# Optimization experiments

Hardware: AMD Instinct MI355X
Metric: run time of the kernel (lower is better)

Reference implementation:

```python
import jax, jax.numpy as jnp
import numpy as np

T, B, COV, H, L = 512, 256, 128, 512, 2
N_DIST_PARAMS = 2  # lnormal


def setup_inputs() -> dict:
    key = jax.random.key(0)
    ks = jax.random.split(key, 20)
    d = {}
    d["x"] = jax.random.normal(ks[0], (T, B, COV + 1), jnp.float32)
    lengths = jax.random.randint(ks[1], (B,), 2, T + 1)
    lengths = -jnp.sort(-lengths)  # packed sequences: descending lengths
    lengths = lengths.at[0].set(T)  # ensure max length == T
    d["lengths"] = lengths
    d["h0"] = jax.random.normal(ks[2], (L, B, H), jnp.float32)
    s = 1.0 / np.sqrt(H)
    in_dims = [COV + 1, H]
    for l in range(L):
        d[f"Wih{l}"] = jax.random.uniform(ks[3 + 4 * l], (3 * H, in_dims[l]), jnp.float32, -s, s)
        d[f"Whh{l}"] = jax.random.uniform(ks[4 + 4 * l], (3 * H, H), jnp.float32, -s, s)
        d[f"bih{l}"] = jax.random.uniform(ks[5 + 4 * l], (3 * H,), jnp.float32, -s, s)
        d[f"bhh{l}"] = jax.random.uniform(ks[6 + 4 * l], (3 * H,), jnp.float32, -s, s)
    sc = 1.0 / np.sqrt(H + 1)
    d["W_cov"] = jax.random.uniform(ks[11], (COV, H + 1), jnp.float32, -sc, sc)
    d["b_cov"] = jax.random.uniform(ks[12], (COV,), jnp.float32, -sc, sc)
    sp = 1.0 / np.sqrt(L * H)
    d["W_par"] = jax.random.uniform(ks[13], (N_DIST_PARAMS, L * H), jnp.float32, -sp, sp)
    d["b_par"] = jax.random.uniform(ks[14], (N_DIST_PARAMS,), jnp.float32, -sp, sp)
    return d


def gru_layer(x, h0, lengths, Wih, Whh, bih, bhh):
    # x: [T, B, D]; h0: [B, H]. PyTorch GRU gate math, masked for ragged lengths
    gi = jnp.einsum('tbd,gd->tbg', x, Wih) + bih  # [T, B, 3H], one big GEMM
    tt = jnp.arange(x.shape[0])

    def step(h, inp):
        gi_t, t = inp
        gh = h @ Whh.T + bhh
        i_r, i_z, i_n = jnp.split(gi_t, 3, axis=-1)
        h_r, h_z, h_n = jnp.split(gh, 3, axis=-1)
        r = jax.nn.sigmoid(i_r + h_r)
        z = jax.nn.sigmoid(i_z + h_z)
        n = jnp.tanh(i_n + r * h_n)
        h_new = (1.0 - z) * n + z * h
        valid = (t < lengths)[:, None]
        h = jnp.where(valid, h_new, h)          # freeze carry past length
        out = jnp.where(valid, h_new, 0.0)       # pad_packed_sequence zero-pads
        return h, out

    h_last, outs = jax.lax.scan(step, h0, (gi, tt))
    return outs, h_last


def reference(x, lengths, h0, Wih0, Whh0, bih0, bhh0, Wih1, Whh1, bih1, bhh1, W_cov, b_cov, W_par, b_par):
    o0, hl0 = gru_layer(x, h0[0], lengths, Wih0, Whh0, bih0, bhh0)
    o1, hl1 = gru_layer(o0, h0[1], lengths, Wih1, Whh1, bih1, bhh1)
    hs = jnp.transpose(o1, (1, 0, 2))  # [B, T, H]
    times = x[:, :, 0].T               # [B, T]
    hwt = jnp.concatenate([hs, times[..., None]], axis=-1)  # [B, T, H+1]
    Tm = x.shape[0]
    # batched masked matmul replacing per-(batch, timestep) GEMV loop
    preds = jnp.einsum('bth,ch->btc', hwt[:, :Tm - 1], W_cov) + b_cov  # [B, T-1, COV]
    mask = (jnp.arange(Tm - 1)[None, :] < (lengths - 1)[:, None])[..., None]
    preds = jnp.where(mask, preds, 0.0)
    # original writes COV values into a COV+1 wide zero buffer; last channel stays 0
    preds = jnp.concatenate([preds, jnp.zeros(preds.shape[:2] + (1,), preds.dtype)], axis=-1)
    last_hidden = jnp.stack([hl0, hl1])                      # [L, B, H]
    last_flat = jnp.reshape(last_hidden, (last_hidden.shape[1], -1))  # torch .view semantics
    dist_params = last_flat @ W_par.T + b_par
    return preds, jnp.exp(-dist_params)
```

## Files before the change

kernel.cpp:

```cpp
#include <hip/hip_runtime.h>


typedef unsigned short u16;
typedef unsigned long long u64;
typedef __attribute__((ext_vector_type(8))) short short8;
typedef short8 bf16x8;
typedef __attribute__((ext_vector_type(4))) float f32x4;

#define T_DIM 512
#define B_DIM 256
#define H_DIM 512
#define G3H   1536
#define BT    131072
#define XPK   256
#define PRED_ELEMS 16875264

#define GLD16(gp, lp) __builtin_amdgcn_global_load_lds( \
    (const __attribute__((address_space(1))) void*)(gp), \
    (__attribute__((address_space(3))) void*)(lp), 16, 0, 0)

__device__ __forceinline__ u16 f2bf(float f) {
    union { float f; unsigned i; } v; v.f = f;
    unsigned i = v.i;
    return (u16)((i + 0x7FFFu + ((i >> 16) & 1u)) >> 16);
}
__device__ __forceinline__ float bf2f(u16 u) {
    union { unsigned i; float f; } v; v.i = ((unsigned)u) << 16; return v.f;
}
__device__ __forceinline__ float sigm(float x) { return 1.f / (1.f + __expf(-x)); }
__device__ __forceinline__ float tanh_f(float x) {
    float ax = fabsf(x);
    float e = __expf(-2.f * ax);
    float t = (1.f - e) / (1.f + e);
    return x < 0.f ? -t : t;
}
__device__ __forceinline__ bf16x8 aload16(const u16* p) {
    union { bf16x8 v; u64 q[2]; } r;
    const u64* qp = (const u64*)p;
    r.q[0] = __hip_atomic_load(qp + 0, __ATOMIC_RELAXED, __HIP_MEMORY_SCOPE_AGENT);
    r.q[1] = __hip_atomic_load(qp + 1, __ATOMIC_RELAXED, __HIP_MEMORY_SCOPE_AGENT);
    return r.v;
}
__device__ __forceinline__ unsigned chk8(bf16x8 v) {
    union { bf16x8 v; unsigned d[4]; } u; u.v = v;
    unsigned b = 0;
#pragma unroll
    for (int i = 0; i < 4; ++i) {
        unsigned d = u.d[i] ^ 0x7FC07FC0u;
        b |= (unsigned)((d & 0xFFFFu) == 0u) | (unsigned)((d >> 16) == 0u);
    }
    return b;
}

__global__ void prep_kernel(const float* __restrict__ Wih0, const float* __restrict__ Wih1,
                            const float* __restrict__ Whh0, const float* __restrict__ Whh1,
                            const float* __restrict__ h0,   const float* __restrict__ Wcov,
                            const float* __restrict__ x,
                            u16* __restrict__ wih0b, u16* __restrict__ wih1b,
                            u16* __restrict__ whh0b, u16* __restrict__ whh1b,
                            u16* __restrict__ h0bf,  u16* __restrict__ wcovb,
                            float* __restrict__ wlastf, u16* __restrict__ xbfc,
                            u16* __restrict__ o0c, u16* __restrict__ o1c, int TC) {
    const int gid = blockIdx.x * 256 + threadIdx.x;
    const int gsz = gridDim.x * 256;
    for (int i = gid; i < 128; i += gsz) wlastf[i] = Wcov[i * 513 + 512];
    for (int i = gid; i < 128 * 512; i += gsz) {
        int r = i >> 9, c = i & 511;
        wcovb[i] = f2bf(Wcov[r * 513 + c]);
    }
    for (int i = gid; i < 512 * 512; i += gsz) h0bf[i] = f2bf(h0[i]);
    for (int i = gid; i < 1536 * XPK; i += gsz) {
        int r = i >> 8, c = i & 255;
        wih0b[i] = f2bf(c < 129 ? Wih0[r * 129 + c] : 0.f);
    }
    for (int i = gid; i < 1536 * 512; i += gsz) wih1b[i] = f2bf(Wih1[i]);
    for (int i = gid; i < 1536 * 512; i += gsz) whh0b[i] = f2bf(Whh0[i]);
    for (int i = gid; i < 1536 * 512; i += gsz) whh1b[i] = f2bf(Whh1[i]);
    {
        const int n = TC * 256 * 256;
        for (int i = gid; i < n; i += gsz) {
            const int row = i >> 8, col = i & 255;
            float v = (col < 129) ? x[(size_t)row * 129 + col] : 0.f;
            xbfc[i] = f2bf(v);
        }
    }
    const u64 SQ = 0x7FC07FC07FC07FC0ULL;
    const size_t nq = (size_t)TC * BT / 4;
    u64* p0 = (u64*)o0c;
    u64* p1 = (u64*)o1c;
    for (size_t i = gid; i < nq; i += gsz) p0[i] = SQ;
    for (size_t i = gid; i < nq; i += gsz) p1[i] = SQ;
}

__global__ void sentinel_kernel(u16* __restrict__ buf, int TC) {
    const u64 SQ = 0x7FC07FC07FC07FC0ULL;
    const size_t nq = (size_t)TC * BT / 4;
    u64* p = (u64*)buf;
    const size_t gid = blockIdx.x * 256 + threadIdx.x;
    const size_t gsz = (size_t)gridDim.x * 256;
    for (size_t i = gid; i < nq; i += gsz) p[i] = SQ;
}

__global__ void cvt_pad_x_kernel(const float* __restrict__ src,
                                 u16* __restrict__ dst, int rows) {
    const int n = rows * 256;
    for (int idx = blockIdx.x * blockDim.x + threadIdx.x; idx < n;
         idx += gridDim.x * blockDim.x) {
        const int row = idx >> 8, col = idx & 255;
        float v = (col < 129) ? src[(size_t)row * 129 + col] : 0.f;
        dst[idx] = f2bf(v);
    }
}

template<int AK>
__global__ __launch_bounds__(256, 2) void scan_fused_kernel(
    const u16* __restrict__ xin,
    const u16* __restrict__ Wih,
    const float* __restrict__ bih,
    const u16* __restrict__ Whh,
    const float* __restrict__ bhh,
    const int* __restrict__ lengths,
    const float* __restrict__ h0l,
    const u16* __restrict__ h0bfl,
    u16* __restrict__ o,
    u16* __restrict__ hcarry,
    float* __restrict__ hlast,
    int t0, int TC) {
    __shared__ __attribute__((aligned(16))) u16 Wl[48 * 520];
    __shared__ __attribute__((aligned(16))) float P[16 * 256];
    __shared__ __attribute__((aligned(16))) float bRZ[32], bNX[16], bNH[16];
    const int tid = threadIdx.x, lane = tid & 63, w = tid >> 6;
    const int n0 = blockIdx.x * 16, b0 = blockIdx.y * 16;
    const int am = lane & 15, aq = lane >> 4;
    constexpr int KW = AK / 4;
    constexpr int KB2 = KW / 32;
#pragma unroll
    for (int it = 0; it < 12; ++it) {
        int f = it * 2048 + tid * 8;
        int j = f >> 9, k = f & 511;
        *(short8*)&Wl[j * 520 + k] =
            *(const short8*)(Whh + ((size_t)((j >> 4) * 512 + n0 + (j & 15))) * 512 + k);
    }
    if (tid < 32) bRZ[tid] = bih[(tid >> 4) * 512 + n0 + (tid & 15)] +
                             bhh[(tid >> 4) * 512 + n0 + (tid & 15)];
    else if (tid < 48) bNX[tid - 32] = bih[1024 + n0 + (tid - 32)];
    else if (tid < 64) bNH[tid - 48] = bhh[1024 + n0 + (tid - 48)];
    bf16x8 wf[3][KB2];
#pragma unroll
    for (int g = 0; g < 3; ++g)
#pragma unroll
        for (int kb = 0; kb < KB2; ++kb)
            wf[g][kb] = *(const short8*)(Wih +
                (size_t)(g * 512 + n0 + am) * AK + w * KW + kb * 32 + aq * 8);
    const int m = tid >> 4, c = tid & 15;
    const int b = b0 + m, col = n0 + c;
    float h = (t0 == 0) ? h0l[(size_t)b * 512 + col]
                        : hlast[(size_t)b * 512 + col];
    const int len = lengths[b];
    bf16x8 xa[KB2], xn[KB2];
#pragma unroll
    for (int kb = 0; kb < KB2; ++kb)
        xa[kb] = *(const short8*)(xin + (size_t)(b0 + am) * AK + w * KW + kb * 32 + aq * 8);
    __syncthreads();
    for (int tl = 0; tl < TC; ++tl) {
        const int t = t0 + tl;
        const u16* Asrc = (tl == 0) ? ((t0 == 0) ? h0bfl : hcarry)
                                    : (o + (size_t)(tl - 1) * BT);
        const u16* arow = Asrc + (size_t)(b0 + am) * 512 + w * 128 + aq * 8;
        bf16x8 av[4];
        if (tl == 0) {
            av[0] = aload16(arow);      av[1] = aload16(arow + 32);
            av[2] = aload16(arow + 64); av[3] = aload16(arow + 96);
        } else {
            for (;;) {
                av[0] = aload16(arow);
                if (!__any((int)chk8(av[0]))) break;
                __builtin_amdgcn_s_sleep(1);
            }
            for (;;) {
                av[1] = aload16(arow + 32);
                av[2] = aload16(arow + 64);
                av[3] = aload16(arow + 96);
                if (!__any((int)(chk8(av[1]) | chk8(av[2]) | chk8(av[3])))) break;
                __builtin_amdgcn_s_sleep(1);
            }
        }
        f32x4 ar = {}, az = {}, anx = {}, anh = {};
#pragma unroll
        for (int kb = 0; kb < KB2; ++kb) {
            ar  = __builtin_amdgcn_mfma_f32_16x16x32_bf16(xa[kb], wf[0][kb], ar, 0, 0, 0);
            az  = __builtin_amdgcn_mfma_f32_16x16x32_bf16(xa[kb], wf[1][kb], az, 0, 0, 0);
            anx = __builtin_amdgcn_mfma_f32_16x16x32_bf16(xa[kb], wf[2][kb], anx, 0, 0, 0);
        }
#pragma unroll
        for (int kb = 0; kb < 4; ++kb) {
            const int k = w * 128 + kb * 32 + aq * 8;
            bf16x8 wr = *(short8*)&Wl[(0 + am) * 520 + k];
            bf16x8 wz = *(short8*)&Wl[(16 + am) * 520 + k];
            bf16x8 wn = *(short8*)&Wl[(32 + am) * 520 + k];
            ar  = __builtin_amdgcn_mfma_f32_16x16x32_bf16(av[kb], wr, ar, 0, 0, 0);
            az  = __builtin_amdgcn_mfma_f32_16x16x32_bf16(av[kb], wz, az, 0, 0, 0);
            anh = __builtin_amdgcn_mfma_f32_16x16x32_bf16(av[kb], wn, anh, 0, 0, 0);
        }
        if (tl < TC - 1) {
#pragma unroll
            for (int kb = 0; kb < KB2; ++kb)
                xn[kb] = *(const short8*)(xin +
                    ((size_t)(tl + 1) * 256 + b0 + am) * AK + w * KW + kb * 32 + aq * 8);
        }
#pragma unroll
        for (int r = 0; r < 4; ++r) {
            P[(w * 4 + 0) * 256 + (aq * 4 + r) * 16 + am] = ar[r];
            P[(w * 4 + 1) * 256 + (aq * 4 + r) * 16 + am] = az[r];
            P[(w * 4 + 2) * 256 + (aq * 4 + r) * 16 + am] = anx[r];
            P[(w * 4 + 3) * 256 + (aq * 4 + r) * 16 + am] = anh[r];
        }
        __syncthreads();
        float Cr = bRZ[c], Cz = bRZ[16 + c], Nx = bNX[c], Nh = bNH[c];
#pragma unroll
        for (int w2 = 0; w2 < 4; ++w2) {
            Cr += P[(w2 * 4 + 0) * 256 + tid];
            Cz += P[(w2 * 4 + 1) * 256 + tid];
            Nx += P[(w2 * 4 + 2) * 256 + tid];
            Nh += P[(w2 * 4 + 3) * 256 + tid];
        }
        __syncthreads();
        float r_ = sigm(Cr);
        float z_ = sigm(Cz);
        float n_ = tanh_f(Nx + r_ * Nh);
        float hnew = (1.f - z_) * n_ + z_ * h;
        h = (t < len) ? hnew : h;
        unsigned hb = (unsigned)f2bf(h);
        unsigned part = hb | ((unsigned)__shfl_down((int)hb, 1) << 16);
        unsigned hi2 = (unsigned)__shfl_down((int)part, 2);
        if ((lane & 3) == 0) {
            u64 q = (u64)part | ((u64)hi2 << 32);
            const int mrow = w * 4 + (lane >> 4);
            const int cg = lane & 15;
            __hip_atomic_store(
                (u64*)(o + (size_t)tl * BT + (size_t)(b0 + mrow) * 512 + n0 + cg),
                q, __ATOMIC_RELAXED, __HIP_MEMORY_SCOPE_AGENT);
        }
        if (tl < TC - 1) {
#pragma unroll
            for (int kb = 0; kb < KB2; ++kb) xa[kb] = xn[kb];
        } else {
            hcarry[(size_t)b * 512 + col] = f2bf(h);
            hlast[(size_t)b * 512 + col] = h;
        }
    }
}

__global__ __launch_bounds__(256) void preds_kernel(
    const u16* __restrict__ o1c, const u16* __restrict__ WcovBf,
    const float* __restrict__ wlastf, const float* __restrict__ bcov,
    const float* __restrict__ x, const int* __restrict__ lengths,
    float* __restrict__ out, int t0) {
    __shared__ __attribute__((aligned(16))) u16 Sh[2][16384];
    const int tid = threadIdx.x, lane = tid & 63, w = tid >> 6;
    const int m0 = blockIdx.x * 128;
    const int r0 = (w & 1) * 64, c0 = (w >> 1) * 64;
    const int am = lane & 15, aq = lane >> 4;
    const int l8 = lane >> 3, lc = lane & 7;
    const int swz = (lc ^ l8) << 3;
    f32x4 acc[4][4] = {};
#pragma unroll
    for (int s = 0; s < 4; ++s) {
        const int i = w * 4 + s, row = i * 8 + l8;
        GLD16(o1c + (size_t)(m0 + row) * 512 + swz, &Sh[0][i * 512]);
        GLD16(WcovBf + (size_t)row * 512 + swz, &Sh[0][8192 + i * 512]);
    }
    __syncthreads();
    int cur = 0;
    for (int kt = 0; kt < 8; ++kt) {
        if (kt + 1 < 8) {
            const int kb = (kt + 1) << 6;
#pragma unroll
            for (int s = 0; s < 4; ++s) {
                const int i = w * 4 + s, row = i * 8 + l8;
                GLD16(o1c + (size_t)(m0 + row) * 512 + kb + swz,
                      &Sh[cur ^ 1][i * 512]);
                GLD16(WcovBf + (size_t)row * 512 + kb + swz,
                      &Sh[cur ^ 1][8192 + i * 512]);
            }
        }
        const u16* Ash = &Sh[cur][0];
        const u16* Bsh = &Sh[cur][8192];
#pragma unroll
        for (int ks = 0; ks < 2; ++ks) {
            bf16x8 a[4], bb[4];
#pragma unroll
            for (int f = 0; f < 4; ++f) {
                const int ar2 = r0 + f * 16 + am;
                a[f] = *(short8*)&Ash[ar2 * 64 + (((ks * 4 + aq) ^ (ar2 & 7)) << 3)];
            }
#pragma unroll
            for (int f = 0; f < 4; ++f) {
                const int br = c0 + f * 16 + am;
                bb[f] = *(short8*)&Bsh[br * 64 + (((ks * 4 + aq) ^ (br & 7)) << 3)];
            }
#pragma unroll
            for (int fi = 0; fi < 4; ++fi)
#pragma unroll
                for (int fj = 0; fj < 4; ++fj)
                    acc[fi][fj] = __builtin_amdgcn_mfma_f32_16x16x32_bf16(
                        a[fi], bb[fj], acc[fi][fj], 0, 0, 0);
        }
        __syncthreads();
        cur ^= 1;
    }
    const int tl = m0 >> 8;
    const int t = t0 + tl;
    if (t < 511) {
#pragma unroll
        for (int fj = 0; fj < 4; ++fj) {
            const int cc = c0 + fj * 16 + am;
            const float bc = bcov[cc], wl = wlastf[cc];
#pragma unroll
            for (int fi = 0; fi < 4; ++fi) {
#pragma unroll
                for (int r = 0; r < 4; ++r) {
                    const int row = m0 + r0 + fi * 16 + aq * 4 + r;
                    const int b = row & 255;
                    const bool valid = t < lengths[b] - 1;
                    const float tim = x[(size_t)t * (256 * 129) + b * 129];
                    out[(size_t)b * (511 * 129) + (size_t)t * 129 + cc] =
                        valid ? acc[fi][fj][r] + bc + tim * wl : 0.f;
                }
            }
        }
        if (tid < 128)
            out[(size_t)((m0 & 255) + tid) * (511 * 129) + (size_t)t * 129 + 128] = 0.f;
    }
}

__global__ void dist_kernel(const float* __restrict__ hl0,
                            const float* __restrict__ hl1,
                            const float* __restrict__ Wpar,
                            const float* __restrict__ bpar, float* __restrict__ out) {
    const int w = threadIdx.x >> 6, lane = threadIdx.x & 63;
    const float bp0 = bpar[0], bp1 = bpar[1];
    for (int rr = 0; rr < 8; ++rr) {
        const int i = (blockIdx.x * 4 + w) * 8 + rr;
        const int l = i >> 7, bb = (2 * i) & 255;
        const float* base = (l ? hl1 : hl0) + (size_t)bb * 512;
        float a0 = 0.f, a1 = 0.f;
#pragma unroll
        for (int cc = 0; cc < 16; ++cc) {
            const int k = cc * 64 + lane;
            const float v = base[k];
            a0 += v * Wpar[k];
            a1 += v * Wpar[1024 + k];
        }
#pragma unroll
        for (int off = 32; off; off >>= 1) {
            a0 += __shfl_down(a0, off);
            a1 += __shfl_down(a1, off);
        }
        if (lane == 0) {
            out[PRED_ELEMS + i * 2 + 0] = __expf(-(a0 + bp0));
            out[PRED_ELEMS + i * 2 + 1] = __expf(-(a1 + bp1));
        }
    }
}

extern "C" void kernel_launch(void* const* d_in, const int* in_sizes, int n_in,
                              void* d_out, int out_size, void* d_ws, size_t ws_size,
                              hipStream_t stream) {
    const float* x    = (const float*)d_in[0];
    const int* lens   = (const int*)d_in[1];
    const float* h0   = (const float*)d_in[2];
    const float* Wih0 = (const float*)d_in[3];
    const float* Whh0 = (const float*)d_in[4];
    const float* bih0 = (const float*)d_in[5];
    const float* bhh0 = (const float*)d_in[6];
    const float* Wih1 = (const float*)d_in[7];
    const float* Whh1 = (const float*)d_in[8];
    const float* bih1 = (const float*)d_in[9];
    const float* bhh1 = (const float*)d_in[10];
    const float* Wcov = (const float*)d_in[11];
    const float* bcov = (const float*)d_in[12];
    const float* Wpar = (const float*)d_in[13];
    const float* bpar = (const float*)d_in[14];
    float* out = (float*)d_out;
    char* wsb = (char*)d_ws;

    size_t off = 0;
    auto take = [&](size_t bytes) -> size_t {
        size_t r = off; off += (bytes + 255) & ~(size_t)255; return r;
    };
    const size_t oHl0   = take((size_t)BT * 4);
    const size_t oHl1   = take((size_t)BT * 4);
    const size_t oHc0   = take((size_t)BT * 2);
    const size_t oHc1   = take((size_t)BT * 2);
    const size_t oH0bf  = take((size_t)2 * BT * 2);
    const size_t oWih0b = take((size_t)G3H * XPK * 2);
    const size_t oWih1b = take((size_t)G3H * 512 * 2);
    const size_t oWhh0b = take((size_t)G3H * 512 * 2);
    const size_t oWhh1b = take((size_t)G3H * 512 * 2);
    const size_t oWcovb = take((size_t)128 * 512 * 2);
    const size_t oWlast = take(512);
    const size_t fixed = off;

    const size_t per = (size_t)256 * XPK * 2 +
                       2 * (size_t)256 * 512 * 2 + 2048;
    const size_t remain = ws_size > fixed ? ws_size - fixed : 0;
    int TC = 1;
    const int cands[10] = {512, 256, 128, 64, 32, 16, 8, 4, 2, 1};
    for (int i = 0; i < 10; ++i)
        if ((size_t)cands[i] * per <= remain) { TC = cands[i]; break; }

    const size_t oXbf = take((size_t)TC * 256 * XPK * 2);
    const size_t oO0  = take((size_t)TC * 256 * 512 * 2);
    const size_t oO1  = take((size_t)TC * 256 * 512 * 2);

    float* hl0  = (float*)(wsb + oHl0);
    float* hl1  = (float*)(wsb + oHl1);
    u16* hcar0  = (u16*)(wsb + oHc0);
    u16* hcar1  = (u16*)(wsb + oHc1);
    u16* h0bf   = (u16*)(wsb + oH0bf);
    u16* wih0b  = (u16*)(wsb + oWih0b);
    u16* wih1b  = (u16*)(wsb + oWih1b);
    u16* whh0b  = (u16*)(wsb + oWhh0b);
    u16* whh1b  = (u16*)(wsb + oWhh1b);
    u16* wcovb  = (u16*)(wsb + oWcovb);
    float* wlastf = (float*)(wsb + oWlast);
    u16* xbfc   = (u16*)(wsb + oXbf);
    u16* o0c    = (u16*)(wsb + oO0);
    u16* o1c    = (u16*)(wsb + oO1);

    prep_kernel<<<1024, 256, 0, stream>>>(Wih0, Wih1, Whh0, Whh1, h0, Wcov, x,
                                          wih0b, wih1b, whh0b, whh1b, h0bf,
                                          wcovb, wlastf, xbfc, o0c, o1c, TC);

    for (int t0 = 0; t0 < T_DIM; t0 += TC) {
        if (t0 > 0) {
            int n = TC * 256 * XPK;
            int pg = (n + 255) / 256; if (pg > 2048) pg = 2048;
            cvt_pad_x_kernel<<<pg, 256, 0, stream>>>(
                x + (size_t)t0 * 256 * 129, xbfc, TC * 256);
            sentinel_kernel<<<2048, 256, 0, stream>>>(o0c, TC);
        }
        scan_fused_kernel<XPK><<<dim3(32, 16), 256, 0, stream>>>(
            xbfc, wih0b, bih0, whh0b, bhh0, lens, h0, h0bf,
            o0c, hcar0, hl0, t0, TC);
        if (t0 > 0)
            sentinel_kernel<<<2048, 256, 0, stream>>>(o1c, TC);
        scan_fused_kernel<512><<<dim3(32, 16), 256, 0, stream>>>(
            o0c, wih1b, bih1, whh1b, bhh1, lens, h0 + (size_t)BT,
            h0bf + (size_t)BT, o1c, hcar1, hl1, t0, TC);
        preds_kernel<<<dim3(TC * 2), 256, 0, stream>>>(
            o1c, wcovb, wlastf, bcov, x, lens, out, t0);
    }
    dist_kernel<<<8, 256, 0, stream>>>(hl0, hl1, Wpar, bpar, out);
}
```

Baseline: 4.425 ms.

## Fuse both GRU layer scans into one wavefront-pipelined dual-layer kernel

```diff
diff --git a/kernel.cpp b/kernel.cpp
--- a/kernel.cpp
+++ b/kernel.cpp
@@ -112,141 +112,275 @@
     }
 }
 
-template<int AK>
-__global__ __launch_bounds__(256, 2) void scan_fused_kernel(
-    const u16* __restrict__ xin,
-    const u16* __restrict__ Wih,
-    const float* __restrict__ bih,
-    const u16* __restrict__ Whh,
-    const float* __restrict__ bhh,
+__global__ __launch_bounds__(512, 2) void scan_dual_kernel(
+    const u16* __restrict__ xbf,
+    const u16* __restrict__ wih0,
+    const float* __restrict__ bih0, const float* __restrict__ bhh0,
+    const u16* __restrict__ wih1,
+    const float* __restrict__ bih1, const float* __restrict__ bhh1,
+    const u16* __restrict__ whh0,
+    const u16* __restrict__ whh1,
     const int* __restrict__ lengths,
-    const float* __restrict__ h0l,
-    const u16* __restrict__ h0bfl,
-    u16* __restrict__ o,
-    u16* __restrict__ hcarry,
-    float* __restrict__ hlast,
+    const float* __restrict__ h0f,
+    const u16* __restrict__ h0b,
+    u16* __restrict__ o0,
+    u16* __restrict__ o1,
+    u16* __restrict__ hc0, u16* __restrict__ hc1,
+    float* __restrict__ hl0, float* __restrict__ hl1,
     int t0, int TC) {
-    __shared__ __attribute__((aligned(16))) u16 Wl[48 * 520];
-    __shared__ __attribute__((aligned(16))) float P[16 * 256];
-    __shared__ __attribute__((aligned(16))) float bRZ[32], bNX[16], bNH[16];
+    __shared__ __attribute__((aligned(16))) u16 Wl[2][48 * 520];
+    __shared__ __attribute__((aligned(16))) float P[4 * 4 * 512];
     const int tid = threadIdx.x, lane = tid & 63, w = tid >> 6;
-    const int n0 = blockIdx.x * 16, b0 = blockIdx.y * 16;
+    const int n0 = blockIdx.x * 16, b0 = blockIdx.y * 32;
     const int am = lane & 15, aq = lane >> 4;
-    constexpr int KW = AK / 4;
-    constexpr int KB2 = KW / 32;
-#pragma unroll
-    for (int it = 0; it < 12; ++it) {
-        int f = it * 2048 + tid * 8;
-        int j = f >> 9, k = f & 511;
-        *(short8*)&Wl[j * 520 + k] =
-            *(const short8*)(Whh + ((size_t)((j >> 4) * 512 + n0 + (j & 15))) * 512 + k);
-    }
-    if (tid < 32) bRZ[tid] = bih[(tid >> 4) * 512 + n0 + (tid & 15)] +
-                             bhh[(tid >> 4) * 512 + n0 + (tid & 15)];
-    else if (tid < 48) bNX[tid - 32] = bih[1024 + n0 + (tid - 32)];
-    else if (tid < 64) bNH[tid - 48] = bhh[1024 + n0 + (tid - 48)];
-    bf16x8 wf[3][KB2];
-#pragma unroll
-    for (int g = 0; g < 3; ++g)
-#pragma unroll
-        for (int kb = 0; kb < KB2; ++kb)
-            wf[g][kb] = *(const short8*)(Wih +
-                (size_t)(g * 512 + n0 + am) * AK + w * KW + kb * 32 + aq * 8);
+    const int layer = w >> 2, v = w & 3;
+#pragma unroll
+    for (int l = 0; l < 2; ++l) {
+        const u16* W = l ? whh1 : whh0;
+#pragma unroll
+        for (int it = 0; it < 6; ++it) {
+            int cnt = it * 512 + tid;
+            int j = cnt >> 6, k = (cnt & 63) * 8;
+            *(short8*)&Wl[l][j * 520 + k] =
+                *(const short8*)(W + (size_t)((j >> 4) * 512 + n0 + (j & 15)) * 512 + k);
+        }
+    }
+    bf16x8 wf[3][4];
+    if (layer == 0) {
+#pragma unroll
+        for (int g = 0; g < 3; ++g)
+#pragma unroll
+            for (int kb = 0; kb < 2; ++kb)
+                wf[g][kb] = *(const short8*)(wih0 +
+                    (size_t)(g * 512 + n0 + am) * 256 + v * 64 + kb * 32 + aq * 8);
+    } else {
+#pragma unroll
+        for (int g = 0; g < 3; ++g)
+#pragma unroll
+            for (int kb = 0; kb < 4; ++kb)
+                wf[g][kb] = *(const short8*)(wih1 +
+                    (size_t)(g * 512 + n0 + am) * 512 + v * 128 + kb * 32 + aq * 8);
+    }
     const int m = tid >> 4, c = tid & 15;
     const int b = b0 + m, col = n0 + c;
-    float h = (t0 == 0) ? h0l[(size_t)b * 512 + col]
-                        : hlast[(size_t)b * 512 + col];
     const int len = lengths[b];
-    bf16x8 xa[KB2], xn[KB2];
-#pragma unroll
-    for (int kb = 0; kb < KB2; ++kb)
-        xa[kb] = *(const short8*)(xin + (size_t)(b0 + am) * AK + w * KW + kb * 32 + aq * 8);
+    float h0s = (t0 == 0) ? h0f[(size_t)b * 512 + col] : hl0[(size_t)b * 512 + col];
+    float h1s = (t0 == 0) ? h0f[(size_t)BT + (size_t)b * 512 + col]
+                          : hl1[(size_t)b * 512 + col];
+    const float br0 = bih0[col] + bhh0[col], bz0 = bih0[512 + col] + bhh0[512 + col];
+    const float bx0 = bih0[1024 + col],      bn0 = bhh0[1024 + col];
+    const float br1 = bih1[col] + bhh1[col], bz1 = bih1[512 + col] + bhh1[512 + col];
+    const float bx1 = bih1[1024 + col],      bn1 = bhh1[1024 + col];
     __syncthreads();
-    for (int tl = 0; tl < TC; ++tl) {
-        const int t = t0 + tl;
-        const u16* Asrc = (tl == 0) ? ((t0 == 0) ? h0bfl : hcarry)
-                                    : (o + (size_t)(tl - 1) * BT);
-        const u16* arow = Asrc + (size_t)(b0 + am) * 512 + w * 128 + aq * 8;
-        bf16x8 av[4];
-        if (tl == 0) {
-            av[0] = aload16(arow);      av[1] = aload16(arow + 32);
-            av[2] = aload16(arow + 64); av[3] = aload16(arow + 96);
+    for (int ec = 0; ec <= TC; ++ec) {
+        const bool a0 = ec < TC, a1 = ec >= 1;
+        f32x4 cr[2] = {}, cz[2] = {}, cx[2] = {}, ch[2] = {};
+        if (layer == 0) {
+            if (a0) {
+                bf16x8 xa[2][2], av[2][4];
+#pragma unroll
+                for (int rt = 0; rt < 2; ++rt)
+#pragma unroll
+                    for (int kb = 0; kb < 2; ++kb)
+                        xa[rt][kb] = *(const short8*)(xbf +
+                            ((size_t)ec * 256 + b0 + rt * 16 + am) * 256 + v * 64 + kb * 32 + aq * 8);
+                const u16* Asrc = (ec == 0) ? ((t0 == 0) ? h0b : hc0)
+                                            : (o0 + (size_t)(ec - 1) * BT);
+                const u16* r0p = Asrc + (size_t)(b0 + am) * 512 + v * 128 + aq * 8;
+                const u16* r1p = Asrc + (size_t)(b0 + 16 + am) * 512 + v * 128 + aq * 8;
+                if (ec == 0) {
+#pragma unroll
+                    for (int kb = 0; kb < 4; ++kb) {
+                        av[0][kb] = aload16(r0p + kb * 32);
+                        av[1][kb] = aload16(r1p + kb * 32);
+                    }
+                } else {
+                    for (;;) {
+                        av[0][0] = aload16(r0p);
+                        if (!__any((int)chk8(av[0][0]))) break;
+                        __builtin_amdgcn_s_sleep(1);
+                    }
+                    for (;;) {
+                        av[0][1] = aload16(r0p + 32);
+                        av[0][2] = aload16(r0p + 64);
+                        av[0][3] = aload16(r0p + 96);
+                        av[1][0] = aload16(r1p);
+                        av[1][1] = aload16(r1p + 32);
+                        av[1][2] = aload16(r1p + 64);
+                        av[1][3] = aload16(r1p + 96);
+                        unsigned bad = chk8(av[0][1]) | chk8(av[0][2]) | chk8(av[0][3]) |
+                                       chk8(av[1][0]) | chk8(av[1][1]) | chk8(av[1][2]) |
+                                       chk8(av[1][3]);
+                        if (!__any((int)bad)) break;
+                        __builtin_amdgcn_s_sleep(1);
+                    }
+                }
+#pragma unroll
+                for (int rt = 0; rt < 2; ++rt)
+#pragma unroll
+                    for (int kb = 0; kb < 2; ++kb) {
+                        cr[rt] = __builtin_amdgcn_mfma_f32_16x16x32_bf16(xa[rt][kb], wf[0][kb], cr[rt], 0, 0, 0);
+                        cz[rt] = __builtin_amdgcn_mfma_f32_16x16x32_bf16(xa[rt][kb], wf[1][kb], cz[rt], 0, 0, 0);
+                        cx[rt] = __builtin_amdgcn_mfma_f32_16x16x32_bf16(xa[rt][kb], wf[2][kb], cx[rt], 0, 0, 0);
+                    }
+#pragma unroll
+                for (int kb = 0; kb < 4; ++kb) {
+                    const int k = v * 128 + kb * 32 + aq * 8;
+                    bf16x8 wr = *(short8*)&Wl[0][(0 + am) * 520 + k];
+                    bf16x8 wz = *(short8*)&Wl[0][(16 + am) * 520 + k];
+                    bf16x8 wn = *(short8*)&Wl[0][(32 + am) * 520 + k];
+#pragma unroll
+                    for (int rt = 0; rt < 2; ++rt) {
+                        cr[rt] = __builtin_amdgcn_mfma_f32_16x16x32_bf16(av[rt][kb], wr, cr[rt], 0, 0, 0);
+                        cz[rt] = __builtin_amdgcn_mfma_f32_16x16x32_bf16(av[rt][kb], wz, cz[rt], 0, 0, 0);
+                        ch[rt] = __builtin_amdgcn_mfma_f32_16x16x32_bf16(av[rt][kb], wn, ch[rt], 0, 0, 0);
+                    }
+                }
+            }
         } else {
-            for (;;) {
-                av[0] = aload16(arow);
-                if (!__any((int)chk8(av[0]))) break;
-                __builtin_amdgcn_s_sleep(1);
-            }
-            for (;;) {
-                av[1] = aload16(arow + 32);
-                av[2] = aload16(arow + 64);
-                av[3] = aload16(arow + 96);
-                if (!__any((int)(chk8(av[1]) | chk8(av[2]) | chk8(av[3])))) break;
-                __builtin_amdgcn_s_sleep(1);
-            }
-        }
-        f32x4 ar = {}, az = {}, anx = {}, anh = {};
-#pragma unroll
-        for (int kb = 0; kb < KB2; ++kb) {
-            ar  = __builtin_amdgcn_mfma_f32_16x16x32_bf16(xa[kb], wf[0][kb], ar, 0, 0, 0);
-            az  = __builtin_amdgcn_mfma_f32_16x16x32_bf16(xa[kb], wf[1][kb], az, 0, 0, 0);
-            anx = __builtin_amdgcn_mfma_f32_16x16x32_bf16(xa[kb], wf[2][kb], anx, 0, 0, 0);
-        }
-#pragma unroll
-        for (int kb = 0; kb < 4; ++kb) {
-            const int k = w * 128 + kb * 32 + aq * 8;
-            bf16x8 wr = *(short8*)&Wl[(0 + am) * 520 + k];
-            bf16x8 wz = *(short8*)&Wl[(16 + am) * 520 + k];
-            bf16x8 wn = *(short8*)&Wl[(32 + am) * 520 + k];
-            ar  = __builtin_amdgcn_mfma_f32_16x16x32_bf16(av[kb], wr, ar, 0, 0, 0);
-            az  = __builtin_amdgcn_mfma_f32_16x16x32_bf16(av[kb], wz, az, 0, 0, 0);
-            anh = __builtin_amdgcn_mfma_f32_16x16x32_bf16(av[kb], wn, anh, 0, 0, 0);
-        }
-        if (tl < TC - 1) {
-#pragma unroll
-            for (int kb = 0; kb < KB2; ++kb)
-                xn[kb] = *(const short8*)(xin +
-                    ((size_t)(tl + 1) * 256 + b0 + am) * AK + w * KW + kb * 32 + aq * 8);
-        }
-#pragma unroll
-        for (int r = 0; r < 4; ++r) {
-            P[(w * 4 + 0) * 256 + (aq * 4 + r) * 16 + am] = ar[r];
-            P[(w * 4 + 1) * 256 + (aq * 4 + r) * 16 + am] = az[r];
-            P[(w * 4 + 2) * 256 + (aq * 4 + r) * 16 + am] = anx[r];
-            P[(w * 4 + 3) * 256 + (aq * 4 + r) * 16 + am] = anh[r];
+            if (a1) {
+                const int s1 = ec - 1;
+                bf16x8 xa[2][4], av[2][4];
+                const u16* Asrc = (s1 == 0) ? ((t0 == 0) ? h0b + BT : hc1)
+                                            : (o1 + (size_t)(s1 - 1) * BT);
+                const u16* r0p = Asrc + (size_t)(b0 + am) * 512 + v * 128 + aq * 8;
+                const u16* r1p = Asrc + (size_t)(b0 + 16 + am) * 512 + v * 128 + aq * 8;
+                if (s1 == 0) {
+#pragma unroll
+                    for (int kb = 0; kb < 4; ++kb) {
+                        av[0][kb] = aload16(r0p + kb * 32);
+                        av[1][kb] = aload16(r1p + kb * 32);
+                    }
+                } else {
+                    for (;;) {
+#pragma unroll
+                        for (int kb = 0; kb < 4; ++kb) {
+                            av[0][kb] = aload16(r0p + kb * 32);
+                            av[1][kb] = aload16(r1p + kb * 32);
+                        }
+                        unsigned bad = 0;
+#pragma unroll
+                        for (int kb = 0; kb < 4; ++kb)
+                            bad |= chk8(av[0][kb]) | chk8(av[1][kb]);
+                        if (!__any((int)bad)) break;
+                        __builtin_amdgcn_s_sleep(1);
+                    }
+                }
+                const u16* xb = o0 + (size_t)s1 * BT;
+                const u16* x0p = xb + (size_t)(b0 + am) * 512 + v * 128 + aq * 8;
+                const u16* x1p = xb + (size_t)(b0 + 16 + am) * 512 + v * 128 + aq * 8;
+                for (;;) {
+#pragma unroll
+                    for (int kb = 0; kb < 4; ++kb) {
+                        xa[0][kb] = aload16(x0p + kb * 32);
+                        xa[1][kb] = aload16(x1p + kb * 32);
+                    }
+                    unsigned bad = 0;
+#pragma unroll
+                    for (int kb = 0; kb < 4; ++kb)
+                        bad |= chk8(xa[0][kb]) | chk8(xa[1][kb]);
+                    if (!__any((int)bad)) break;
+                    __builtin_amdgcn_s_sleep(1);
+                }
+#pragma unroll
+                for (int kb = 0; kb < 4; ++kb) {
+                    const int k = v * 128 + kb * 32 + aq * 8;
+                    bf16x8 wr = *(short8*)&Wl[1][(0 + am) * 520 + k];
+                    bf16x8 wz = *(short8*)&Wl[1][(16 + am) * 520 + k];
+                    bf16x8 wn = *(short8*)&Wl[1][(32 + am) * 520 + k];
+#pragma unroll
+                    for (int rt = 0; rt < 2; ++rt) {
+                        cr[rt] = __builtin_amdgcn_mfma_f32_16x16x32_bf16(xa[rt][kb], wf[0][kb], cr[rt], 0, 0, 0);
+                        cz[rt] = __builtin_amdgcn_mfma_f32_16x16x32_bf16(xa[rt][kb], wf[1][kb], cz[rt], 0, 0, 0);
+                        cx[rt] = __builtin_amdgcn_mfma_f32_16x16x32_bf16(xa[rt][kb], wf[2][kb], cx[rt], 0, 0, 0);
+                        cr[rt] = __builtin_amdgcn_mfma_f32_16x16x32_bf16(av[rt][kb], wr, cr[rt], 0, 0, 0);
+                        cz[rt] = __builtin_amdgcn_mfma_f32_16x16x32_bf16(av[rt][kb], wz, cz[rt], 0, 0, 0);
+                        ch[rt] = __builtin_amdgcn_mfma_f32_16x16x32_bf16(av[rt][kb], wn, ch[rt], 0, 0, 0);
+                    }
+                }
+            }
         }
         __syncthreads();
-        float Cr = bRZ[c], Cz = bRZ[16 + c], Nx = bNX[c], Nh = bNH[c];
-#pragma unroll
-        for (int w2 = 0; w2 < 4; ++w2) {
-            Cr += P[(w2 * 4 + 0) * 256 + tid];
-            Cz += P[(w2 * 4 + 1) * 256 + tid];
-            Nx += P[(w2 * 4 + 2) * 256 + tid];
-            Nh += P[(w2 * 4 + 3) * 256 + tid];
+        if (layer == 0 && a0) {
+#pragma unroll
+            for (int rt = 0; rt < 2; ++rt)
+#pragma unroll
+                for (int r = 0; r < 4; ++r) {
+                    const int e = (rt * 16 + aq * 4 + r) * 16 + am;
+                    P[(v * 4 + 0) * 512 + e] = cr[rt][r];
+                    P[(v * 4 + 1) * 512 + e] = cz[rt][r];
+                    P[(v * 4 + 2) * 512 + e] = cx[rt][r];
+                    P[(v * 4 + 3) * 512 + e] = ch[rt][r];
+                }
         }
         __syncthreads();
-        float r_ = sigm(Cr);
-        float z_ = sigm(Cz);
-        float n_ = tanh_f(Nx + r_ * Nh);
-        float hnew = (1.f - z_) * n_ + z_ * h;
-        h = (t < len) ? hnew : h;
-        unsigned hb = (unsigned)f2bf(h);
-        unsigned part = hb | ((unsigned)__shfl_down((int)hb, 1) << 16);
-        unsigned hi2 = (unsigned)__shfl_down((int)part, 2);
-        if ((lane & 3) == 0) {
-            u64 q = (u64)part | ((u64)hi2 << 32);
-            const int mrow = w * 4 + (lane >> 4);
-            const int cg = lane & 15;
-            __hip_atomic_store(
-                (u64*)(o + (size_t)tl * BT + (size_t)(b0 + mrow) * 512 + n0 + cg),
-                q, __ATOMIC_RELAXED, __HIP_MEMORY_SCOPE_AGENT);
-        }
-        if (tl < TC - 1) {
-#pragma unroll
-            for (int kb = 0; kb < KB2; ++kb) xa[kb] = xn[kb];
-        } else {
-            hcarry[(size_t)b * 512 + col] = f2bf(h);
-            hlast[(size_t)b * 512 + col] = h;
+        if (a0) {
+            float Cr = br0, Cz = bz0, Nx = bx0, Nh = bn0;
+#pragma unroll
+            for (int kw = 0; kw < 4; ++kw) {
+                Cr += P[(kw * 4 + 0) * 512 + tid];
+                Cz += P[(kw * 4 + 1) * 512 + tid];
+                Nx += P[(kw * 4 + 2) * 512 + tid];
+                Nh += P[(kw * 4 + 3) * 512 + tid];
+            }
+            float r_ = sigm(Cr), z_ = sigm(Cz);
+            float n_ = tanh_f(Nx + r_ * Nh);
+            float hnew = (1.f - z_) * n_ + z_ * h0s;
+            h0s = (t0 + ec < len) ? hnew : h0s;
+            unsigned hb = (unsigned)f2bf(h0s);
+            unsigned part = hb | ((unsigned)__shfl_down((int)hb, 1) << 16);
+            unsigned hi2 = (unsigned)__shfl_down((int)part, 2);
+            if ((lane & 3) == 0) {
+                u64 q = (u64)part | ((u64)hi2 << 32);
+                __hip_atomic_store(
+                    (u64*)(o0 + (size_t)ec * BT + (size_t)b * 512 + col),
+                    q, __ATOMIC_RELAXED, __HIP_MEMORY_SCOPE_AGENT);
+            }
+            if (ec == TC - 1) {
+                hc0[(size_t)b * 512 + col] = f2bf(h0s);
+                hl0[(size_t)b * 512 + col] = h0s;
+            }
+        }
+        __syncthreads();
+        if (layer == 1 && a1) {
+#pragma unroll
+            for (int rt = 0; rt < 2; ++rt)
+#pragma unroll
+                for (int r = 0; r < 4; ++r) {
+                    const int e = (rt * 16 + aq * 4 + r) * 16 + am;
+                    P[(v * 4 + 0) * 512 + e] = cr[rt][r];
+                    P[(v * 4 + 1) * 512 + e] = cz[rt][r];
+                    P[(v * 4 + 2) * 512 + e] = cx[rt][r];
+                    P[(v * 4 + 3) * 512 + e] = ch[rt][r];
+                }
+        }
+        __syncthreads();
+        if (a1) {
+            float Cr = br1, Cz = bz1, Nx = bx1, Nh = bn1;
+#pragma unroll
+            for (int kw = 0; kw < 4; ++kw) {
+                Cr += P[(kw * 4 + 0) * 512 + tid];
+                Cz += P[(kw * 4 + 1) * 512 + tid];
+                Nx += P[(kw * 4 + 2) * 512 + tid];
+                Nh += P[(kw * 4 + 3) * 512 + tid];
+            }
+            float r_ = sigm(Cr), z_ = sigm(Cz);
+            float n_ = tanh_f(Nx + r_ * Nh);
+            float hnew = (1.f - z_) * n_ + z_ * h1s;
+            h1s = (t0 + ec - 1 < len) ? hnew : h1s;
+            unsigned hb = (unsigned)f2bf(h1s);
+            unsigned part = hb | ((unsigned)__shfl_down((int)hb, 1) << 16);
+            unsigned hi2 = (unsigned)__shfl_down((int)part, 2);
+            if ((lane & 3) == 0) {
+                u64 q = (u64)part | ((u64)hi2 << 32);
+                __hip_atomic_store(
+                    (u64*)(o1 + (size_t)(ec - 1) * BT + (size_t)b * 512 + col),
+                    q, __ATOMIC_RELAXED, __HIP_MEMORY_SCOPE_AGENT);
+            }
+            if (ec == TC) {
+                hc1[(size_t)b * 512 + col] = f2bf(h1s);
+                hl1[(size_t)b * 512 + col] = h1s;
+            }
         }
     }
 }
@@ -440,15 +574,11 @@
             cvt_pad_x_kernel<<<pg, 256, 0, stream>>>(
                 x + (size_t)t0 * 256 * 129, xbfc, TC * 256);
             sentinel_kernel<<<2048, 256, 0, stream>>>(o0c, TC);
-        }
-        scan_fused_kernel<XPK><<<dim3(32, 16), 256, 0, stream>>>(
-            xbfc, wih0b, bih0, whh0b, bhh0, lens, h0, h0bf,
-            o0c, hcar0, hl0, t0, TC);
-        if (t0 > 0)
             sentinel_kernel<<<2048, 256, 0, stream>>>(o1c, TC);
-        scan_fused_kernel<512><<<dim3(32, 16), 256, 0, stream>>>(
-            o0c, wih1b, bih1, whh1b, bhh1, lens, h0 + (size_t)BT,
-            h0bf + (size_t)BT, o1c, hcar1, hl1, t0, TC);
+        }
+        scan_dual_kernel<<<dim3(32, 8), 512, 0, stream>>>(
+            xbfc, wih0b, bih0, bhh0, wih1b, bih1, bhh1, whh0b, whh1b,
+            lens, h0, h0bf, o0c, o1c, hcar0, hcar1, hl0, hl1, t0, TC);
         preds_kernel<<<dim3(TC * 2), 256, 0, stream>>>(
             o1c, wcovb, wlastf, bcov, x, lens, out, t0);
     }
```

New measurement: 4.790 ms. 8.3% more time.
